# Kernel optimization log

Hardware: AMD Instinct MI355X
Metric: run time of the kernel (lower is better)

## Reference

```python
import jax, jax.numpy as jnp
import numpy as np

NEG_SLOPE = 0.2

def setup_inputs() -> dict:
    key = jax.random.key(0)
    k1, k2, k3, k4, k5 = jax.random.split(key, 5)
    B, N, Fin, Fout, H = 4, 2048, 256, 128, 4
    h = jax.random.normal(k1, (B, N, Fin), dtype=jnp.float32)
    adj = jax.random.randint(k2, (N, N), 0, 2, dtype=jnp.int32)
    W_w = jax.random.normal(k3, (Fout, Fin), dtype=jnp.float32) * (1.414 / np.sqrt(Fin))
    W_b = jax.random.normal(k4, (Fout,), dtype=jnp.float32) * 0.01
    attn_w = jax.random.normal(k5, (H, 2 * Fout), dtype=jnp.float32) * (1.414 / np.sqrt(2 * Fout))
    return {"h": h, "adj": adj, "W_w": W_w, "W_b": W_b, "attn_w": attn_w}

def reference(h, adj, W_w, W_b, attn_w):
    Fout = W_w.shape[0]
    # Wh: [B, N, Fout]
    Wh = jnp.einsum('bnf,of->bno', h, W_w) + W_b
    a_left = attn_w[:, :Fout]   # [H, Fout]
    a_right = attn_w[:, Fout:]  # [H, Fout]
    e_left = jnp.einsum('bno,ho->bhn', Wh, a_left)   # [B, H, N]
    e_right = jnp.einsum('bno,ho->bhn', Wh, a_right)  # [B, H, N]
    # additive broadcast score: [B, H, N, N]
    e = e_left[:, :, :, None] + e_right[:, :, None, :]
    e = jnp.where(e > 0, e, NEG_SLOPE * e)  # LeakyReLU(0.2)
    mask = (adj == 0)[None, None, :, :]     # [1,1,N,N] broadcast over B,H
    e = jnp.where(mask, -jnp.inf, e)
    attn = jax.nn.softmax(e, axis=-1)
    attn = jnp.where(jnp.isnan(attn), 0.0, attn)
    # h_prime: [B, H, N, Fout]
    h_prime = jnp.einsum('bhij,bjo->bhio', attn, Wh)
    out = jnp.mean(h_prime, axis=1)
    return jax.nn.relu(out)
```

## Files before the change

### kernel.cpp

```cpp
#include <hip/hip_runtime.h>
#include <stdint.h>

#define BB 4
#define NN 2048
#define FIN 256
#define FOUT 128
#define NH 4
#define NEG_SLOPE 0.2f

typedef short bf16x8 __attribute__((ext_vector_type(8)));
typedef unsigned short u16x8 __attribute__((ext_vector_type(8)));
typedef float f32x4 __attribute__((ext_vector_type(4)));
typedef unsigned long long u64;

__device__ inline float b2f(unsigned short u) {
    union { unsigned int i; float f; } x; x.i = ((unsigned int)u) << 16; return x.f;
}
__device__ inline unsigned short f2b(float f) {
    union { float f; unsigned int i; } x; x.f = f;
    unsigned int r = x.i + 0x7fffu + ((x.i >> 16) & 1u);
    return (unsigned short)(r >> 16);
}
__device__ inline unsigned short f2b_fast(float f) {
    union { float f; unsigned int i; } x; x.f = f;
    return (unsigned short)((x.i + 0x8000u) >> 16);
}
union F16U { unsigned short u; _Float16 h; };
__device__ inline float f16lo(unsigned int v) { F16U x; x.u = (unsigned short)(v & 0xffffu); return (float)x.h; }
__device__ inline float f16hi(unsigned int v) { F16U x; x.u = (unsigned short)(v >> 16); return (float)x.h; }
__device__ inline unsigned int packf16(float a, float b) {
    F16U x, y; x.h = (_Float16)a; y.h = (_Float16)b;
    return (unsigned int)x.u | ((unsigned int)y.u << 16);
}

__global__ __launch_bounds__(256) void kcvt_w(const float* __restrict__ Ww,
                                              unsigned short* __restrict__ Whi,
                                              unsigned short* __restrict__ Wlo) {
    int idx = blockIdx.x * 256 + threadIdx.x;
    float v = Ww[idx];
    unsigned short hb = f2b(v);
    Whi[idx] = hb;
    Wlo[idx] = f2b(v - b2f(hb));
}

__global__ __launch_bounds__(256) void k1_wh(
    const float* __restrict__ h, const unsigned short* __restrict__ Whi,
    const unsigned short* __restrict__ Wlo, const float* __restrict__ Wb,
    const float* __restrict__ attw, unsigned short* __restrict__ WhT,
    float2* __restrict__ ELpair, unsigned int* __restrict__ ERpk) {
    __shared__ unsigned short Ahi[16][264];
    __shared__ unsigned short Alo[16][264];
    __shared__ float whs[16][132];
    int t = threadIdx.x;
    int b = blockIdx.x >> 7;
    int n0 = (blockIdx.x & 127) * 16;
    {
        int r = t >> 4, c = (t & 15) * 16;
        const float* hp = h + ((size_t)(b * NN + n0 + r)) * FIN + c;
        u16x8 hi0, hi1, lo0, lo1;
        #pragma unroll
        for (int q = 0; q < 4; ++q) {
            float4 v = *(const float4*)(hp + q * 4);
            float vv[4] = {v.x, v.y, v.z, v.w};
            #pragma unroll
            for (int e = 0; e < 4; ++e) {
                int idx = q * 4 + e;
                unsigned short hb = f2b(vv[e]);
                unsigned short lb = f2b(vv[e] - b2f(hb));
                if (idx < 8) { hi0[idx] = (short)hb; lo0[idx] = (short)lb; }
                else         { hi1[idx - 8] = (short)hb; lo1[idx - 8] = (short)lb; }
            }
        }
        *(u16x8*)&Ahi[r][c] = *(u16x8*)&hi0;
        *(u16x8*)&Ahi[r][c + 8] = *(u16x8*)&hi1;
        *(u16x8*)&Alo[r][c] = *(u16x8*)&lo0;
        *(u16x8*)&Alo[r][c + 8] = *(u16x8*)&lo1;
    }
    __syncthreads();
    int lane = t & 63, wv = t >> 6;
    int m = lane & 15, quad = lane >> 4;
    int o0 = wv * 32;
    f32x4 acc0 = {0.f, 0.f, 0.f, 0.f}, acc1 = {0.f, 0.f, 0.f, 0.f};
    const unsigned short* wh0 = Whi + (size_t)(o0 + m) * FIN;
    const unsigned short* wl0 = Wlo + (size_t)(o0 + m) * FIN;
    const unsigned short* wh1 = Whi + (size_t)(o0 + 16 + m) * FIN;
    const unsigned short* wl1 = Wlo + (size_t)(o0 + 16 + m) * FIN;
    #pragma unroll
    for (int ks = 0; ks < 8; ++ks) {
        int ko = ks * 32 + quad * 8;
        bf16x8 ahi = *(bf16x8*)&Ahi[m][ko];
        bf16x8 alo = *(bf16x8*)&Alo[m][ko];
        bf16x8 bh0 = *(const bf16x8*)(wh0 + ko);
        bf16x8 bl0 = *(const bf16x8*)(wl0 + ko);
        bf16x8 bh1 = *(const bf16x8*)(wh1 + ko);
        bf16x8 bl1 = *(const bf16x8*)(wl1 + ko);
        acc0 = __builtin_amdgcn_mfma_f32_16x16x32_bf16(ahi, bh0, acc0, 0, 0, 0);
        acc0 = __builtin_amdgcn_mfma_f32_16x16x32_bf16(ahi, bl0, acc0, 0, 0, 0);
        acc0 = __builtin_amdgcn_mfma_f32_16x16x32_bf16(alo, bh0, acc0, 0, 0, 0);
        acc1 = __builtin_amdgcn_mfma_f32_16x16x32_bf16(ahi, bh1, acc1, 0, 0, 0);
        acc1 = __builtin_amdgcn_mfma_f32_16x16x32_bf16(ahi, bl1, acc1, 0, 0, 0);
        acc1 = __builtin_amdgcn_mfma_f32_16x16x32_bf16(alo, bh1, acc1, 0, 0, 0);
    }
    float bias0 = Wb[o0 + m], bias1 = Wb[o0 + 16 + m];
    #pragma unroll
    for (int reg = 0; reg < 4; ++reg) {
        int row = quad * 4 + reg;
        whs[row][o0 + m] = acc0[reg] + bias0;
        whs[row][o0 + 16 + m] = acc1[reg] + bias1;
    }
    __syncthreads();
    {
        int o = t >> 1, half = t & 1;
        u16x8 v8;
        #pragma unroll
        for (int r = 0; r < 8; ++r) v8[r] = (short)f2b(whs[half * 8 + r][o]);
        *(u16x8*)(WhT + (size_t)(b * FOUT + o) * NN + n0 + half * 8) = v8;
    }
    {
        int outi = t >> 1, half = t & 1;
        int i = outi >> 3, d = outi & 7, hh = d & 3, side = d >> 2;
        const float* arow = attw + hh * (2 * FOUT) + side * FOUT + half * 64;
        float s = 0.f;
        #pragma unroll 8
        for (int k = 0; k < 64; ++k) s = fmaf(whs[i][half * 64 + k], arow[k], s);
        s += __shfl_xor(s, 1);
        if (half == 0) {
            float p = __expf(s), n = __expf(NEG_SLOPE * s);
            if (side == 0) {
                ELpair[(size_t)(b * NH + hh) * NN + n0 + i] = make_float2(p, n);
            } else {
                ERpk[((size_t)b * NN + n0 + i) * NH + hh] = packf16(p, n);
            }
        }
    }
}

__global__ __launch_bounds__(256) void k_pack(const int* __restrict__ adj,
                                              u64* __restrict__ mask) {
    int row = blockIdx.x;
    int wave = threadIdx.x >> 6, lane = threadIdx.x & 63;
    #pragma unroll
    for (int it = 0; it < 8; ++it) {
        int w = it * 4 + wave;
        int j = w * 64 + lane;
        u64 m = __ballot(adj[(size_t)row * NN + j] != 0);
        if (lane == 0) mask[row * 32 + w] = m;
    }
}

__global__ __launch_bounds__(256) void kstat_t(
    const unsigned int* __restrict__ ERpk, const float2* __restrict__ ELpair,
    const u64* __restrict__ mask, float* __restrict__ sPartT) {
    int lane = threadIdx.x & 63, b = threadIdx.x >> 6;
    int i = blockIdx.x * 64 + lane;
    int j0 = blockIdx.y * 64;
    u64 mw = mask[(size_t)i * 32 + (j0 >> 6)];
    float elp[NH], eln[NH], acc[NH];
    #pragma unroll
    for (int hh = 0; hh < NH; ++hh) {
        float2 e2 = ELpair[(size_t)(b * NH + hh) * NN + i];
        elp[hh] = e2.x; eln[hh] = e2.y; acc[hh] = 0.f;
    }
    const uint4* erb = (const uint4*)(ERpk + ((size_t)b * NN + j0) * NH);
    #pragma unroll 8
    for (int jj = 0; jj < 64; ++jj) {
        uint4 er4 = erb[jj];
        bool bit = (mw >> jj) & 1ull;
        float m0 = fmaxf(elp[0] * f16lo(er4.x), eln[0] * f16hi(er4.x));
        float m1 = fmaxf(elp[1] * f16lo(er4.y), eln[1] * f16hi(er4.y));
        float m2 = fmaxf(elp[2] * f16lo(er4.z), eln[2] * f16hi(er4.z));
        float m3 = fmaxf(elp[3] * f16lo(er4.w), eln[3] * f16hi(er4.w));
        acc[0] += bit ? m0 : 0.f;
        acc[1] += bit ? m1 : 0.f;
        acc[2] += bit ? m2 : 0.f;
        acc[3] += bit ? m3 : 0.f;
    }
    #pragma unroll
    for (int hh = 0; hh < NH; ++hh)
        sPartT[(((size_t)blockIdx.y * BB + b) * NH + hh) * NN + i] = acc[hh];
}

__global__ __launch_bounds__(512, 4) void k2b_mfma(
    const unsigned short* __restrict__ WhT, const unsigned int* __restrict__ ERpk,
    const float2* __restrict__ ELpair, const float* __restrict__ sPartT,
    const u64* __restrict__ mask, float* __restrict__ P) {
    __shared__ unsigned short wt[64][264];
    __shared__ u64 mws[64][8];
    __shared__ float elsc_s[64][8];
    int t = threadIdx.x;
    int b = blockIdx.y, i0 = blockIdx.x * 64, jq = blockIdx.z;
    int lane = t & 63, wv = t >> 6;
    int m = lane & 15, quad = lane >> 4;
    if (t < 256) {
        int li = t & 63, hh = t >> 6;
        float s = 0.f;
        #pragma unroll
        for (int jp = 0; jp < 32; ++jp)
            s += sPartT[(((size_t)jp * BB + b) * NH + hh) * NN + i0 + li];
        float iv = (s > 0.f) ? 0.25f / s : 0.f;
        float2 e2 = ELpair[(size_t)(b * NH + hh) * NN + i0 + li];
        elsc_s[li][hh * 2]     = e2.x * iv;
        elsc_s[li][hh * 2 + 1] = e2.y * iv;
    }
    {
        int r = t >> 3, wp = t & 7;
        mws[r][wp] = mask[(size_t)(i0 + r) * 32 + jq * 8 + wp];
    }
    int r0 = wv * 8;
    int o0 = wv * 16;
    const unsigned short* bp = WhT + (size_t)(b * FOUT + o0 + m) * NN + jq * 512;
    f32x4 acc[4];
    #pragma unroll
    for (int k = 0; k < 4; ++k) acc[k] = (f32x4){0.f, 0.f, 0.f, 0.f};

    for (int ch = 0; ch < 2; ++ch) {
        int j0 = ch * 256;
        __syncthreads();
        bf16x8 bfr[8];
        #pragma unroll
        for (int ks = 0; ks < 8; ++ks)
            bfr[ks] = *(const bf16x8*)(bp + j0 + ks * 32 + quad * 8);
        float erp[4][4], ern[4][4];
        #pragma unroll
        for (int q = 0; q < 4; ++q) {
            int jg = jq * 512 + j0 + q * 64 + lane;
            uint4 er4 = *(const uint4*)(ERpk + ((size_t)b * NN + jg) * 4);
            erp[q][0] = f16lo(er4.x); ern[q][0] = f16hi(er4.x);
            erp[q][1] = f16lo(er4.y); ern[q][1] = f16hi(er4.y);
            erp[q][2] = f16lo(er4.z); ern[q][2] = f16hi(er4.z);
            erp[q][3] = f16lo(er4.w); ern[q][3] = f16hi(er4.w);
        }
        #pragma unroll
        for (int r = 0; r < 8; ++r) {
            int ir = r0 + r;
            float4 c0 = *(float4*)&elsc_s[ir][0];
            float4 c1 = *(float4*)&elsc_s[ir][4];
            u64 mwq[4] = {mws[ir][ch * 4 + 0], mws[ir][ch * 4 + 1],
                          mws[ir][ch * 4 + 2], mws[ir][ch * 4 + 3]};
            #pragma unroll
            for (int q = 0; q < 4; ++q) {
                float p = fmaxf(c0.x * erp[q][0], c0.y * ern[q][0]);
                p += fmaxf(c0.z * erp[q][1], c0.w * ern[q][1]);
                p += fmaxf(c1.x * erp[q][2], c1.y * ern[q][2]);
                p += fmaxf(c1.z * erp[q][3], c1.w * ern[q][3]);
                wt[ir][q * 64 + lane] = ((mwq[q] >> lane) & 1ull) ? f2b_fast(p) : 0;
            }
        }
        __syncthreads();
        #pragma unroll
        for (int isub = 0; isub < 4; ++isub) {
            #pragma unroll
            for (int ks = 0; ks < 8; ++ks) {
                bf16x8 a = *(bf16x8*)&wt[isub * 16 + m][ks * 32 + quad * 8];
                acc[isub] = __builtin_amdgcn_mfma_f32_16x16x32_bf16(a, bfr[ks], acc[isub], 0, 0, 0);
            }
        }
    }
    float* pb = P + (((size_t)jq * BB + b) * NN + i0) * FOUT;
    #pragma unroll
    for (int isub = 0; isub < 4; ++isub) {
        #pragma unroll
        for (int reg = 0; reg < 4; ++reg) {
            int row = isub * 16 + quad * 4 + reg;
            pb[(size_t)row * FOUT + o0 + m] = acc[isub][reg];
        }
    }
}

__global__ __launch_bounds__(256) void k3_relu(const float* __restrict__ P,
                                               float* __restrict__ out) {
    int idx = blockIdx.x * 256 + threadIdx.x;
    const int slab = BB * NN * FOUT / 4;
    float4 a = ((const float4*)P)[idx];
    float4 c1 = ((const float4*)P)[idx + slab];
    float4 c2 = ((const float4*)P)[idx + 2 * slab];
    float4 c3 = ((const float4*)P)[idx + 3 * slab];
    a.x = fmaxf(a.x + c1.x + c2.x + c3.x, 0.f);
    a.y = fmaxf(a.y + c1.y + c2.y + c3.y, 0.f);
    a.z = fmaxf(a.z + c1.z + c2.z + c3.z, 0.f);
    a.w = fmaxf(a.w + c1.w + c2.w + c3.w, 0.f);
    ((float4*)out)[idx] = a;
}

extern "C" void kernel_launch(void* const* d_in, const int* in_sizes, int n_in,
                              void* d_out, int out_size, void* d_ws, size_t ws_size,
                              hipStream_t stream) {
    const float* h    = (const float*)d_in[0];
    const int* adj    = (const int*)d_in[1];
    const float* Ww   = (const float*)d_in[2];
    const float* Wb   = (const float*)d_in[3];
    const float* attw = (const float*)d_in[4];
    float* out = (float*)d_out;
    char* ws = (char*)d_ws;
    unsigned short* Whi = (unsigned short*)(ws);
    unsigned short* Wlo = (unsigned short*)(ws + 65536);
    unsigned short* WhT = (unsigned short*)(ws + 131072);
    float2*       ELpair = (float2*)(ws + 2228224);
    unsigned int* ERpk   = (unsigned int*)(ws + 2490368);
    u64*          mask   = (u64*)(ws + 2621440);
    float*        sPartT = (float*)(ws + 3145728);
    float*        P      = (float*)(ws + 7340032);

    kcvt_w<<<dim3(128), dim3(256), 0, stream>>>(Ww, Whi, Wlo);
    k1_wh<<<dim3(BB * NN / 16), dim3(256), 0, stream>>>(h, Whi, Wlo, Wb, attw,
                                                        WhT, ELpair, ERpk);
    k_pack<<<dim3(NN), dim3(256), 0, stream>>>(adj, mask);
    kstat_t<<<dim3(NN / 64, NN / 64), dim3(256), 0, stream>>>(ERpk, ELpair, mask, sPartT);
    k2b_mfma<<<dim3(NN / 64, BB, 4), dim3(512), 0, stream>>>(WhT, ERpk, ELpair,
                                                             sPartT, mask, P);
    k3_relu<<<dim3(BB * NN * FOUT / 1024), dim3(256), 0, stream>>>(P, out);
}
```

Measured before the change: 134.4 us.

## Merge prep kernels, fuse split-K reduction into MFMA kernel, store ER as fp32

```diff
diff --git a/kernel.cpp b/kernel.cpp
--- a/kernel.cpp
+++ b/kernel.cpp
@@ -25,29 +25,39 @@
     union { float f; unsigned int i; } x; x.f = f;
     return (unsigned short)((x.i + 0x8000u) >> 16);
 }
-union F16U { unsigned short u; _Float16 h; };
-__device__ inline float f16lo(unsigned int v) { F16U x; x.u = (unsigned short)(v & 0xffffu); return (float)x.h; }
-__device__ inline float f16hi(unsigned int v) { F16U x; x.u = (unsigned short)(v >> 16); return (float)x.h; }
-__device__ inline unsigned int packf16(float a, float b) {
-    F16U x, y; x.h = (_Float16)a; y.h = (_Float16)b;
-    return (unsigned int)x.u | ((unsigned int)y.u << 16);
-}
-
-__global__ __launch_bounds__(256) void kcvt_w(const float* __restrict__ Ww,
-                                              unsigned short* __restrict__ Whi,
-                                              unsigned short* __restrict__ Wlo) {
-    int idx = blockIdx.x * 256 + threadIdx.x;
-    float v = Ww[idx];
-    unsigned short hb = f2b(v);
-    Whi[idx] = hb;
-    Wlo[idx] = f2b(v - b2f(hb));
+
+__global__ __launch_bounds__(256) void k0_prep(const float* __restrict__ Ww,
+                                               unsigned short* __restrict__ Whi,
+                                               unsigned short* __restrict__ Wlo,
+                                               const int* __restrict__ adj,
+                                               u64* __restrict__ mask,
+                                               int* __restrict__ cnt) {
+    int bid = blockIdx.x;
+    if (bid < 128) {
+        int idx = bid * 256 + threadIdx.x;
+        float v = Ww[idx];
+        unsigned short hb = f2b(v);
+        Whi[idx] = hb;
+        Wlo[idx] = f2b(v - b2f(hb));
+        if (bid == 0 && threadIdx.x < BB * 32) cnt[threadIdx.x] = 0;
+    } else {
+        int row = bid - 128;
+        int wave = threadIdx.x >> 6, lane = threadIdx.x & 63;
+        #pragma unroll
+        for (int it = 0; it < 8; ++it) {
+            int w = it * 4 + wave;
+            int j = w * 64 + lane;
+            u64 m = __ballot(adj[(size_t)row * NN + j] != 0);
+            if (lane == 0) mask[row * 32 + w] = m;
+        }
+    }
 }
 
 __global__ __launch_bounds__(256) void k1_wh(
     const float* __restrict__ h, const unsigned short* __restrict__ Whi,
     const unsigned short* __restrict__ Wlo, const float* __restrict__ Wb,
     const float* __restrict__ attw, unsigned short* __restrict__ WhT,
-    float2* __restrict__ ELpair, unsigned int* __restrict__ ERpk) {
+    float2* __restrict__ ELpair, float2* __restrict__ ERf) {
     __shared__ unsigned short Ahi[16][264];
     __shared__ unsigned short Alo[16][264];
     __shared__ float whs[16][132];
@@ -129,27 +139,14 @@
             if (side == 0) {
                 ELpair[(size_t)(b * NH + hh) * NN + n0 + i] = make_float2(p, n);
             } else {
-                ERpk[((size_t)b * NN + n0 + i) * NH + hh] = packf16(p, n);
+                ERf[((size_t)b * NN + n0 + i) * NH + hh] = make_float2(p, n);
             }
         }
     }
 }
 
-__global__ __launch_bounds__(256) void k_pack(const int* __restrict__ adj,
-                                              u64* __restrict__ mask) {
-    int row = blockIdx.x;
-    int wave = threadIdx.x >> 6, lane = threadIdx.x & 63;
-    #pragma unroll
-    for (int it = 0; it < 8; ++it) {
-        int w = it * 4 + wave;
-        int j = w * 64 + lane;
-        u64 m = __ballot(adj[(size_t)row * NN + j] != 0);
-        if (lane == 0) mask[row * 32 + w] = m;
-    }
-}
-
 __global__ __launch_bounds__(256) void kstat_t(
-    const unsigned int* __restrict__ ERpk, const float2* __restrict__ ELpair,
+    const float2* __restrict__ ERf, const float2* __restrict__ ELpair,
     const u64* __restrict__ mask, float* __restrict__ sPartT) {
     int lane = threadIdx.x & 63, b = threadIdx.x >> 6;
     int i = blockIdx.x * 64 + lane;
@@ -161,15 +158,16 @@
         float2 e2 = ELpair[(size_t)(b * NH + hh) * NN + i];
         elp[hh] = e2.x; eln[hh] = e2.y; acc[hh] = 0.f;
     }
-    const uint4* erb = (const uint4*)(ERpk + ((size_t)b * NN + j0) * NH);
+    const float4* erb = (const float4*)(ERf + ((size_t)b * NN + j0) * NH);
     #pragma unroll 8
     for (int jj = 0; jj < 64; ++jj) {
-        uint4 er4 = erb[jj];
+        float4 e0 = erb[jj * 2];
+        float4 e1 = erb[jj * 2 + 1];
         bool bit = (mw >> jj) & 1ull;
-        float m0 = fmaxf(elp[0] * f16lo(er4.x), eln[0] * f16hi(er4.x));
-        float m1 = fmaxf(elp[1] * f16lo(er4.y), eln[1] * f16hi(er4.y));
-        float m2 = fmaxf(elp[2] * f16lo(er4.z), eln[2] * f16hi(er4.z));
-        float m3 = fmaxf(elp[3] * f16lo(er4.w), eln[3] * f16hi(er4.w));
+        float m0 = fmaxf(elp[0] * e0.x, eln[0] * e0.y);
+        float m1 = fmaxf(elp[1] * e0.z, eln[1] * e0.w);
+        float m2 = fmaxf(elp[2] * e1.x, eln[2] * e1.y);
+        float m3 = fmaxf(elp[3] * e1.z, eln[3] * e1.w);
         acc[0] += bit ? m0 : 0.f;
         acc[1] += bit ? m1 : 0.f;
         acc[2] += bit ? m2 : 0.f;
@@ -181,12 +179,14 @@
 }
 
 __global__ __launch_bounds__(512, 4) void k2b_mfma(
-    const unsigned short* __restrict__ WhT, const unsigned int* __restrict__ ERpk,
+    const unsigned short* __restrict__ WhT, const float2* __restrict__ ERf,
     const float2* __restrict__ ELpair, const float* __restrict__ sPartT,
-    const u64* __restrict__ mask, float* __restrict__ P) {
+    const u64* __restrict__ mask, float* __restrict__ P,
+    int* __restrict__ cnt, float* __restrict__ out) {
     __shared__ unsigned short wt[64][264];
     __shared__ u64 mws[64][8];
     __shared__ float elsc_s[64][8];
+    __shared__ int sOld;
     int t = threadIdx.x;
     int b = blockIdx.y, i0 = blockIdx.x * 64, jq = blockIdx.z;
     int lane = t & 63, wv = t >> 6;
@@ -224,11 +224,12 @@
         #pragma unroll
         for (int q = 0; q < 4; ++q) {
             int jg = jq * 512 + j0 + q * 64 + lane;
-            uint4 er4 = *(const uint4*)(ERpk + ((size_t)b * NN + jg) * 4);
-            erp[q][0] = f16lo(er4.x); ern[q][0] = f16hi(er4.x);
-            erp[q][1] = f16lo(er4.y); ern[q][1] = f16hi(er4.y);
-            erp[q][2] = f16lo(er4.z); ern[q][2] = f16hi(er4.z);
-            erp[q][3] = f16lo(er4.w); ern[q][3] = f16hi(er4.w);
+            const float4* ef = (const float4*)(ERf + ((size_t)b * NN + jg) * NH);
+            float4 e0 = ef[0], e1 = ef[1];
+            erp[q][0] = e0.x; ern[q][0] = e0.y;
+            erp[q][1] = e0.z; ern[q][1] = e0.w;
+            erp[q][2] = e1.x; ern[q][2] = e1.y;
+            erp[q][3] = e1.z; ern[q][3] = e1.w;
         }
         #pragma unroll
         for (int r = 0; r < 8; ++r) {
@@ -265,21 +266,28 @@
             pb[(size_t)row * FOUT + o0 + m] = acc[isub][reg];
         }
     }
-}
-
-__global__ __launch_bounds__(256) void k3_relu(const float* __restrict__ P,
-                                               float* __restrict__ out) {
-    int idx = blockIdx.x * 256 + threadIdx.x;
-    const int slab = BB * NN * FOUT / 4;
-    float4 a = ((const float4*)P)[idx];
-    float4 c1 = ((const float4*)P)[idx + slab];
-    float4 c2 = ((const float4*)P)[idx + 2 * slab];
-    float4 c3 = ((const float4*)P)[idx + 3 * slab];
-    a.x = fmaxf(a.x + c1.x + c2.x + c3.x, 0.f);
-    a.y = fmaxf(a.y + c1.y + c2.y + c3.y, 0.f);
-    a.z = fmaxf(a.z + c1.z + c2.z + c3.z, 0.f);
-    a.w = fmaxf(a.w + c1.w + c2.w + c3.w, 0.f);
-    ((float4*)out)[idx] = a;
+    __threadfence();
+    __syncthreads();
+    if (t == 0) sOld = atomicAdd(&cnt[b * 32 + blockIdx.x], 1);
+    __syncthreads();
+    if (sOld == 3) {
+        __threadfence();
+        const float4* q0 = (const float4*)(P + (((size_t)0 * BB + b) * NN + i0) * FOUT);
+        const float4* q1 = (const float4*)(P + (((size_t)1 * BB + b) * NN + i0) * FOUT);
+        const float4* q2 = (const float4*)(P + (((size_t)2 * BB + b) * NN + i0) * FOUT);
+        const float4* q3 = (const float4*)(P + (((size_t)3 * BB + b) * NN + i0) * FOUT);
+        float4* ov = (float4*)(out + ((size_t)b * NN + i0) * FOUT);
+        #pragma unroll
+        for (int e = 0; e < 4; ++e) {
+            int ii = e * 512 + t;
+            float4 a = q0[ii], b1 = q1[ii], c = q2[ii], d = q3[ii];
+            a.x = fmaxf(a.x + b1.x + c.x + d.x, 0.f);
+            a.y = fmaxf(a.y + b1.y + c.y + d.y, 0.f);
+            a.z = fmaxf(a.z + b1.z + c.z + d.z, 0.f);
+            a.w = fmaxf(a.w + b1.w + c.w + d.w, 0.f);
+            ov[ii] = a;
+        }
+    }
 }
 
 extern "C" void kernel_launch(void* const* d_in, const int* in_sizes, int n_in,
@@ -296,17 +304,16 @@
     unsigned short* Wlo = (unsigned short*)(ws + 65536);
     unsigned short* WhT = (unsigned short*)(ws + 131072);
     float2*       ELpair = (float2*)(ws + 2228224);
-    unsigned int* ERpk   = (unsigned int*)(ws + 2490368);
-    u64*          mask   = (u64*)(ws + 2621440);
-    float*        sPartT = (float*)(ws + 3145728);
-    float*        P      = (float*)(ws + 7340032);
-
-    kcvt_w<<<dim3(128), dim3(256), 0, stream>>>(Ww, Whi, Wlo);
+    float2*       ERf    = (float2*)(ws + 2490368);
+    u64*          mask   = (u64*)(ws + 2752512);
+    float*        sPartT = (float*)(ws + 3276800);
+    float*        P      = (float*)(ws + 7471104);
+    int*          cnt    = (int*)(ws + 24248320);
+
+    k0_prep<<<dim3(128 + NN), dim3(256), 0, stream>>>(Ww, Whi, Wlo, adj, mask, cnt);
     k1_wh<<<dim3(BB * NN / 16), dim3(256), 0, stream>>>(h, Whi, Wlo, Wb, attw,
-                                                        WhT, ELpair, ERpk);
-    k_pack<<<dim3(NN), dim3(256), 0, stream>>>(adj, mask);
-    kstat_t<<<dim3(NN / 64, NN / 64), dim3(256), 0, stream>>>(ERpk, ELpair, mask, sPartT);
-    k2b_mfma<<<dim3(NN / 64, BB, 4), dim3(512), 0, stream>>>(WhT, ERpk, ELpair,
-                                                             sPartT, mask, P);
-    k3_relu<<<dim3(BB * NN * FOUT / 1024), dim3(256), 0, stream>>>(P, out);
-}
+                                                        WhT, ELpair, ERf);
+    kstat_t<<<dim3(NN / 64, NN / 64), dim3(256), 0, stream>>>(ERf, ELpair, mask, sPartT);
+    k2b_mfma<<<dim3(NN / 64, BB, 4), dim3(512), 0, stream>>>(WhT, ERf, ELpair,
+                                                             sPartT, mask, P, cnt, out);
+}
```

Result: slower. 262.3 us (+95.1%).
